# Kernel tuning notes

Measured on AMD Instinct MI355X. Metric: run time of the kernel, lower is better.

Reference implementation:

```python
import jax, jax.numpy as jnp
import numpy as np

D_MODEL = 512
D_ALPHA = 100
D_PH = 80
SCALE = 1.0 / np.sqrt(D_MODEL)


def gru_cell(x, h, Wih, Whh, bih, bhh):
    # PyTorch GRU gate order: r, z, n
    gi = x @ Wih.T + bih
    gh = h @ Whh.T + bhh
    ir, iz, inn = jnp.split(gi, 3, axis=-1)
    hr, hz, hn = jnp.split(gh, 3, axis=-1)
    r = jax.nn.sigmoid(ir + hr)
    z = jax.nn.sigmoid(iz + hz)
    n = jnp.tanh(inn + r * hn)
    return (1.0 - z) * n + z * h


def attend(q, k, v):
    # q: [B,D], k/v: [B,L,D]
    scores = jnp.einsum('bd,bld->bl', q, k) * SCALE
    a = jax.nn.softmax(scores, axis=-1)  # [B,L]
    o = jnp.einsum('bl,bld->bd', a, v)
    return a, o


def setup_inputs() -> dict:
    key = jax.random.key(0)
    ks = jax.random.split(key, 25)
    D = D_MODEL

    def u(k, shape, fan):
        return jax.random.uniform(k, shape, jnp.float32, -1.0, 1.0) / np.sqrt(fan)

    inp = {
        'text': jax.random.randint(ks[0], (256, 128), 0, D_ALPHA),
        'tgt': jax.random.randint(ks[1], (256, 64), 0, D_PH),
        'E_alpha': jax.random.normal(ks[2], (D_ALPHA, D), jnp.float32),
        'enc_Wih_f': u(ks[3], (3 * D, D), D),
        'enc_Whh_f': u(ks[4], (3 * D, D), D),
        'enc_bih_f': u(ks[5], (3 * D,), D),
        'enc_bhh_f': u(ks[6], (3 * D,), D),
        'enc_Wih_b': u(ks[7], (3 * D, D), D),
        'enc_Whh_b': u(ks[8], (3 * D, D), D),
        'enc_bih_b': u(ks[9], (3 * D,), D),
        'enc_bhh_b': u(ks[10], (3 * D,), D),
        'hpost_W': u(ks[11], (D, 2 * D), 2 * D),
        'hpost_b': u(ks[12], (D,), 2 * D),
        'wk_W': u(ks[13], (D, 2 * D), 2 * D),
        'wk_b': u(ks[14], (D,), 2 * D),
        'wv_W': u(ks[15], (D, 2 * D), 2 * D),
        'wv_b': u(ks[16], (D,), 2 * D),
        'E_ph': jax.random.normal(ks[17], (D_PH, D), jnp.float32),
        'dec_Wih': u(ks[18], (3 * D, 2 * D), 2 * D),
        'dec_Whh': u(ks[19], (3 * D, D), D),
        'dec_bih': u(ks[20], (3 * D,), D),
        'dec_bhh': u(ks[21], (3 * D,), D),
        'post_W': u(ks[22], (D_PH, D), D),
        'post_b': u(ks[23], (D_PH,), D),
    }
    return inp


def reference(text, tgt, E_alpha, enc_Wih_f, enc_Whh_f, enc_bih_f, enc_bhh_f,
              enc_Wih_b, enc_Whh_b, enc_bih_b, enc_bhh_b, hpost_W, hpost_b,
              wk_W, wk_b, wv_W, wv_b, E_ph, dec_Wih, dec_Whh, dec_bih,
              dec_bhh, post_W, post_b):
    B, LT = text.shape
    LP = tgt.shape[1]

    # ---- Encoder: bidirectional single-layer GRU (eval: dropout = identity)
    emb = E_alpha[text]                     # [B,LT,D]
    xs = jnp.swapaxes(emb, 0, 1)            # [LT,B,D]
    h0 = jnp.zeros((B, D_MODEL), emb.dtype)

    def mk_step(Wih, Whh, bih, bhh):
        def step(h, x):
            h2 = gru_cell(x, h, Wih, Whh, bih, bhh)
            return h2, h2
        return step

    hF, ysF = jax.lax.scan(mk_step(enc_Wih_f, enc_Whh_f, enc_bih_f, enc_bhh_f), h0, xs)
    hB, ysB = jax.lax.scan(mk_step(enc_Wih_b, enc_Whh_b, enc_bih_b, enc_bhh_b), h0, xs[::-1])
    ysB = ysB[::-1]
    enc_o = jnp.swapaxes(jnp.concatenate([ysF, ysB], axis=-1), 0, 1)  # [B,LT,2D]
    h = jnp.tanh(jnp.concatenate([hF, hB], axis=-1) @ hpost_W.T + hpost_b)  # [B,D]

    k = enc_o @ wk_W.T + wk_b               # [B,LT,D]
    v = enc_o @ wv_W.T + wv_b               # [B,LT,D]

    # ---- initial attention from encoder hidden; eval-mode first token is argmax
    # over tgt[:,0] reshaped to [B,1,1], i.e. always index 0.
    a_sl0, a_o0 = attend(h, k, v)
    dec_i0 = jnp.zeros((B,), jnp.int32)

    def dstep(carry, _):
        hh, a_o, a_sl, dec_i = carry
        e = E_ph[dec_i]                                  # [B,D]
        x = gru_cell(jnp.concatenate([e, a_o], axis=-1), hh,
                     dec_Wih, dec_Whh, dec_bih, dec_bhh)  # [B,D]
        o = x @ post_W.T + post_b                         # [B,D_PH]
        n_sl, n_o = attend(x, k, v)
        nxt = jnp.argmax(o, axis=-1).astype(jnp.int32)
        return (x, n_o, n_sl, nxt), (a_sl, o)

    _, (attn_t, res_t) = jax.lax.scan(dstep, (h, a_o0, a_sl0, dec_i0), None, length=LP)
    attn = jnp.swapaxes(attn_t, 0, 1)        # [B,LP,LT]
    res = jnp.swapaxes(res_t, 0, 1)          # [B,LP,D_PH]
    return attn, res
```

## Files before the change

### kernel.cpp

```cpp
#include <hip/hip_runtime.h>
#include <math.h>

#define B   256
#define LT  128
#define LP  64
#define DM  512
#define D3  1536
#define DPH 80
#define SCALE_F 0.044194173824159216f

__device__ __forceinline__ float dot4(float4 a, float4 b) {
    return a.x*b.x + a.y*b.y + a.z*b.z + a.w*b.w;
}
__device__ __forceinline__ float sigmoidf_(float x) {
    return 1.0f / (1.0f + expf(-x));
}

__global__ __launch_bounds__(256) void precompG_kernel(
    const float* __restrict__ Emb, const float* __restrict__ W,
    const float* __restrict__ bias, float* __restrict__ G,
    int wstride, int woff)
{
    const int n  = blockIdx.x * 256 + threadIdx.x;
    const int r0 = blockIdx.y * 4;
    __shared__ float es[4][DM];
    for (int i = threadIdx.x; i < 4 * DM; i += 256)
        es[i >> 9][i & 511] = Emb[(r0 + (i >> 9)) * DM + (i & 511)];
    __syncthreads();
    float acc[4] = {0.f, 0.f, 0.f, 0.f};
    const float* wr = &W[(size_t)n * wstride + woff];
    for (int j = 0; j < DM; j += 4) {
        float4 w4 = *(const float4*)&wr[j];
        #pragma unroll
        for (int rr = 0; rr < 4; ++rr) {
            float4 e4 = *(const float4*)&es[rr][j];
            acc[rr] += dot4(e4, w4);
        }
    }
    float bv = bias[n];
    #pragma unroll
    for (int rr = 0; rr < 4; ++rr)
        G[(r0 + rr) * D3 + n] = acc[rr] + bv;
}

__global__ __launch_bounds__(256) void enc_step_kernel(
    const float* __restrict__ Gf, const float* __restrict__ Gb,
    const float* __restrict__ Whh_f, const float* __restrict__ Whh_b,
    const float* __restrict__ bhh_f, const float* __restrict__ bhh_b,
    const int* __restrict__ text,
    const float* __restrict__ hF_in, float* __restrict__ hF_out,
    const float* __restrict__ hB_in, float* __restrict__ hB_out,
    float* __restrict__ E,
    int s)
{
    const int dir = blockIdx.z;
    const int t   = (dir == 0) ? s : (LT - 1 - s);
    const int yoff = (dir == 0) ? 0 : DM;
    const float* G   = (dir == 0) ? Gf    : Gb;
    const float* Whh = (dir == 0) ? Whh_f : Whh_b;
    const float* bhh = (dir == 0) ? bhh_f : bhh_b;
    const float* hin = (dir == 0) ? hF_in : hB_in;
    float* hout      = (dir == 0) ? hF_out : hB_out;

    __shared__ float As[2][16][36];
    __shared__ float Bs[2][96][36];

    const int tid = threadIdx.x;
    const int jj  = tid & 15;
    const int bb  = tid >> 4;
    const int jtile = blockIdx.x * 32;
    const int btile = blockIdx.y * 16;

    float acc[2][3];
    #pragma unroll
    for (int js = 0; js < 2; ++js)
        #pragma unroll
        for (int g = 0; g < 3; ++g) acc[js][g] = 0.f;

    const int lrow = tid >> 3;
    const int lcol = (tid & 7) * 4;

    int wrow[3];
    #pragma unroll
    for (int rr = 0; rr < 3; ++rr) {
        int brow = lrow + rr * 32;
        wrow[rr] = (brow >> 5) * DM + jtile + (brow & 31);
    }

    float4 rA = make_float4(0.f,0.f,0.f,0.f);
    if (tid < 128)
        rA = *(const float4*)&hin[(btile + lrow) * DM + lcol];
    float4 rB0 = *(const float4*)&Whh[(size_t)wrow[0] * DM + lcol];
    float4 rB1 = *(const float4*)&Whh[(size_t)wrow[1] * DM + lcol];
    float4 rB2 = *(const float4*)&Whh[(size_t)wrow[2] * DM + lcol];

    int buf = 0;
    for (int k = 0; k < 16; ++k) {
        if (tid < 128)
            *(float4*)&As[buf][lrow][lcol] = rA;
        *(float4*)&Bs[buf][lrow][lcol]      = rB0;
        *(float4*)&Bs[buf][lrow + 32][lcol] = rB1;
        *(float4*)&Bs[buf][lrow + 64][lcol] = rB2;
        __syncthreads();
        if (k < 15) {
            const int k0 = (k + 1) * 32;
            if (tid < 128)
                rA = *(const float4*)&hin[(btile + lrow) * DM + k0 + lcol];
            rB0 = *(const float4*)&Whh[(size_t)wrow[0] * DM + k0 + lcol];
            rB1 = *(const float4*)&Whh[(size_t)wrow[1] * DM + k0 + lcol];
            rB2 = *(const float4*)&Whh[(size_t)wrow[2] * DM + k0 + lcol];
        }
        #pragma unroll
        for (int c4 = 0; c4 < 8; ++c4) {
            float4 av = *(float4*)&As[buf][bb][c4 * 4];
            float4 bv[2][3];
            #pragma unroll
            for (int js = 0; js < 2; ++js)
                #pragma unroll
                for (int g = 0; g < 3; ++g)
                    bv[js][g] = *(float4*)&Bs[buf][g * 32 + jj + 16 * js][c4 * 4];
            #pragma unroll
            for (int js = 0; js < 2; ++js)
                #pragma unroll
                for (int g = 0; g < 3; ++g)
                    acc[js][g] += dot4(av, bv[js][g]);
        }
        buf ^= 1;
    }

    const int b = btile + bb;
    const int c = text[b * LT + t];
    #pragma unroll
    for (int js = 0; js < 2; ++js) {
        const int j = jtile + jj + 16 * js;
        float hr = acc[js][0] + bhh[j];
        float hz = acc[js][1] + bhh[DM + j];
        float hn = acc[js][2] + bhh[2 * DM + j];
        float r = sigmoidf_(G[c * D3 + j] + hr);
        float z = sigmoidf_(G[c * D3 + DM + j] + hz);
        float n = tanhf(G[c * D3 + 2 * DM + j] + r * hn);
        float hp = hin[b * DM + j];
        float hv = (1.f - z) * n + z * hp;
        hout[b * DM + j] = hv;
        E[(size_t)(b * LT + t) * 1024 + yoff + j] = hv;
    }
}

__global__ __launch_bounds__(256) void kv_chunk_kernel(
    const float* __restrict__ E,
    const float* __restrict__ wk, const float* __restrict__ wv,
    const float* __restrict__ kb, const float* __restrict__ vb,
    float* __restrict__ T, int r0)
{
    __shared__ float As[64][36];
    __shared__ float Bk[64][36];
    __shared__ float Bv[64][36];
    const int tid = threadIdx.x;
    const int nn = tid & 15, bb = tid >> 4;
    const int ntile = blockIdx.x * 64;
    const int mtile = blockIdx.y * 64;

    float ak[4][4], av_[4][4];
    #pragma unroll
    for (int m = 0; m < 4; ++m)
        #pragma unroll
        for (int i = 0; i < 4; ++i) { ak[m][i] = 0.f; av_[m][i] = 0.f; }

    const int lrow = tid >> 3;
    const int lcol = (tid & 7) * 4;

    for (int k0 = 0; k0 < 1024; k0 += 32) {
        __syncthreads();
        *(float4*)&As[lrow][lcol] =
            *(const float4*)&E[(size_t)(r0 + mtile + lrow) * 1024 + k0 + lcol];
        *(float4*)&As[lrow + 32][lcol] =
            *(const float4*)&E[(size_t)(r0 + mtile + lrow + 32) * 1024 + k0 + lcol];
        *(float4*)&Bk[lrow][lcol] =
            *(const float4*)&wk[(ntile + lrow) * 1024 + k0 + lcol];
        *(float4*)&Bk[lrow + 32][lcol] =
            *(const float4*)&wk[(ntile + lrow + 32) * 1024 + k0 + lcol];
        *(float4*)&Bv[lrow][lcol] =
            *(const float4*)&wv[(ntile + lrow) * 1024 + k0 + lcol];
        *(float4*)&Bv[lrow + 32][lcol] =
            *(const float4*)&wv[(ntile + lrow + 32) * 1024 + k0 + lcol];
        __syncthreads();
        #pragma unroll
        for (int c4 = 0; c4 < 8; ++c4) {
            float4 a4[4], k4[4], v4[4];
            #pragma unroll
            for (int m = 0; m < 4; ++m) a4[m] = *(float4*)&As[bb + 16 * m][c4 * 4];
            #pragma unroll
            for (int i = 0; i < 4; ++i) {
                k4[i] = *(float4*)&Bk[nn + 16 * i][c4 * 4];
                v4[i] = *(float4*)&Bv[nn + 16 * i][c4 * 4];
            }
            #pragma unroll
            for (int m = 0; m < 4; ++m)
                #pragma unroll
                for (int i = 0; i < 4; ++i) {
                    ak[m][i]  += dot4(a4[m], k4[i]);
                    av_[m][i] += dot4(a4[m], v4[i]);
                }
        }
    }
    #pragma unroll
    for (int m = 0; m < 4; ++m) {
        const int lm = mtile + bb + 16 * m;
        #pragma unroll
        for (int i = 0; i < 4; ++i) {
            const int gn = ntile + nn + 16 * i;
            T[(size_t)lm * 1024 + gn]       = ak[m][i]  + kb[gn];
            T[(size_t)lm * 1024 + DM + gn]  = av_[m][i] + vb[gn];
        }
    }
}

__global__ __launch_bounds__(256) void copy4_kernel(
    float4* __restrict__ dst, const float4* __restrict__ src, int n4)
{
    int i = blockIdx.x * 256 + threadIdx.x;
    const int stride = gridDim.x * 256;
    for (; i < n4; i += stride) dst[i] = src[i];
}

__global__ __launch_bounds__(256) void hpost_kernel(
    const float* __restrict__ hF, const float* __restrict__ hB,
    const float* __restrict__ W, const float* __restrict__ bias,
    float* __restrict__ out)
{
    const int b = blockIdx.x;
    __shared__ float as_[1024];
    for (int i = threadIdx.x; i < DM; i += 256) {
        as_[i]      = hF[b * DM + i];
        as_[DM + i] = hB[b * DM + i];
    }
    __syncthreads();
    for (int n = threadIdx.x; n < DM; n += 256) {
        const float* wr = &W[n * 1024];
        float acc = 0.f;
        for (int j = 0; j < 1024; j += 4)
            acc += dot4(*(const float4*)&as_[j], *(const float4*)&wr[j]);
        out[b * DM + n] = tanhf(acc + bias[n]);
    }
}

__global__ __launch_bounds__(256) void dec_step_kernel(
    const float* __restrict__ Gd,
    const float* __restrict__ dec_Wih, const float* __restrict__ dec_Whh,
    const float* __restrict__ bhh,
    const int* __restrict__ dec_i,
    const float* __restrict__ a_o,
    const float* __restrict__ h_in, float* __restrict__ h_out)
{
    __shared__ float As[2][8][36];
    __shared__ float Bs[2][96][36];
    const int tid = threadIdx.x;
    const int jj = tid & 15;
    const int js = (tid >> 4) & 1;
    const int bb = tid >> 5;
    const int jtile = blockIdx.x * 32;
    const int btile = blockIdx.y * 8;

    float acc[4];
    #pragma unroll
    for (int g = 0; g < 4; ++g) acc[g] = 0.f;

    const int lrow = tid >> 3;
    const int lcol = (tid & 7) * 4;

    int wrow[3];
    #pragma unroll
    for (int rr = 0; rr < 3; ++rr) {
        int brow = lrow + rr * 32;
        wrow[rr] = (brow >> 5) * DM + jtile + (brow & 31);
    }

    float4 rA = make_float4(0.f,0.f,0.f,0.f), rB0, rB1, rB2;
    if (tid < 64)
        rA = *(const float4*)&a_o[(btile + lrow) * DM + lcol];
    rB0 = *(const float4*)&dec_Wih[(size_t)wrow[0] * 1024 + DM + lcol];
    rB1 = *(const float4*)&dec_Wih[(size_t)wrow[1] * 1024 + DM + lcol];
    rB2 = *(const float4*)&dec_Wih[(size_t)wrow[2] * 1024 + DM + lcol];

    int buf = 0;
    for (int kk = 0; kk < 32; ++kk) {
        const int phase = kk >> 4;
        if (tid < 64)
            *(float4*)&As[buf][lrow][lcol] = rA;
        *(float4*)&Bs[buf][lrow][lcol]      = rB0;
        *(float4*)&Bs[buf][lrow + 32][lcol] = rB1;
        *(float4*)&Bs[buf][lrow + 64][lcol] = rB2;
        __syncthreads();
        if (kk < 31) {
            const int nk = kk + 1;
            const int np = nk >> 4;
            const int k0 = (nk & 15) * 32;
            if (tid < 64) {
                const float* Aptr = (np == 0) ? a_o : h_in;
                rA = *(const float4*)&Aptr[(btile + lrow) * DM + k0 + lcol];
            }
            if (np == 0) {
                rB0 = *(const float4*)&dec_Wih[(size_t)wrow[0] * 1024 + DM + k0 + lcol];
                rB1 = *(const float4*)&dec_Wih[(size_t)wrow[1] * 1024 + DM + k0 + lcol];
                rB2 = *(const float4*)&dec_Wih[(size_t)wrow[2] * 1024 + DM + k0 + lcol];
            } else {
                rB0 = *(const float4*)&dec_Whh[(size_t)wrow[0] * DM + k0 + lcol];
                rB1 = *(const float4*)&dec_Whh[(size_t)wrow[1] * DM + k0 + lcol];
                rB2 = *(const float4*)&dec_Whh[(size_t)wrow[2] * DM + k0 + lcol];
            }
        }
        #pragma unroll
        for (int c4 = 0; c4 < 8; ++c4) {
            float4 av = *(float4*)&As[buf][bb][c4 * 4];
            float4 bv[3];
            #pragma unroll
            for (int g = 0; g < 3; ++g)
                bv[g] = *(float4*)&Bs[buf][g * 32 + jj + 16 * js][c4 * 4];
            acc[0]         += dot4(av, bv[0]);
            acc[1]         += dot4(av, bv[1]);
            acc[2 + phase] += dot4(av, bv[2]);
        }
        buf ^= 1;
    }

    const int b = btile + bb;
    const int c = dec_i[b];
    const int j = jtile + jj + 16 * js;
    float r = sigmoidf_(Gd[c * D3 + j] + bhh[j] + acc[0]);
    float z = sigmoidf_(Gd[c * D3 + DM + j] + bhh[DM + j] + acc[1]);
    float n = tanhf(Gd[c * D3 + 2 * DM + j] + acc[2]
                    + r * (acc[3] + bhh[2 * DM + j]));
    float hp = h_in[b * DM + j];
    h_out[b * DM + j] = (1.f - z) * n + z * hp;
}

__global__ __launch_bounds__(256) void dec_attend_post_kernel(
    const float* __restrict__ q,
    const float* __restrict__ EKV,
    const float* __restrict__ post_W, const float* __restrict__ post_b,
    float* __restrict__ attn, float* __restrict__ res,
    float* __restrict__ a_o, int* __restrict__ dec_i,
    int s, int attn_row, int do_post, int do_attn)
{
    const int b = blockIdx.x;
    const int tid = threadIdx.x;
    __shared__ float qs[DM];
    __shared__ float part[256];
    __shared__ float sarr[LT];
    __shared__ float red[2];
    __shared__ float4 pvp[2][128];

    if (tid < 128)
        *(float4*)&qs[tid * 4] = *(const float4*)&q[b * DM + tid * 4];
    __syncthreads();

    if (do_post) {
        if (tid < DPH) {
            const float* wr = &post_W[tid * DM];
            float acc = 0.f;
            for (int d = 0; d < DM; d += 4)
                acc += dot4(*(const float4*)&qs[d], *(const float4*)&wr[d]);
            float lv = acc + post_b[tid];
            res[(b * LP + s) * DPH + tid] = lv;
            part[tid] = lv;
        }
        __syncthreads();
        if (tid == 0) {
            float best = part[0]; int bi = 0;
            for (int p = 1; p < DPH; ++p) {
                float vv = part[p];
                if (vv > best) { best = vv; bi = p; }
            }
            dec_i[b] = bi;
        }
        __syncthreads();
    }

    if (do_attn) {
        {
            const int r = tid & 127, half = tid >> 7;
            const float* kr = &EKV[(size_t)(b * LT + r) * 1024 + half * 256];
            const float* qh = &qs[half * 256];
            float p = 0.f;
            #pragma unroll
            for (int d = 0; d < 256; d += 4)
                p += dot4(*(const float4*)&qh[d], *(const float4*)&kr[d]);
            part[tid] = p;
        }
        __syncthreads();
        if (tid < LT) sarr[tid] = (part[tid] + part[tid + 128]) * SCALE_F;
        __syncthreads();
        if (tid < 64) {
            float m = fmaxf(sarr[tid], sarr[tid + 64]);
            #pragma unroll
            for (int off = 32; off > 0; off >>= 1)
                m = fmaxf(m, __shfl_xor(m, off));
            if (tid == 0) red[0] = m;
        }
        __syncthreads();
        const float smax = red[0];
        if (tid < LT) sarr[tid] = expf(sarr[tid] - smax);
        __syncthreads();
        if (tid < 64) {
            float ssum = sarr[tid] + sarr[tid + 64];
            #pragma unroll
            for (int off = 32; off > 0; off >>= 1)
                ssum += __shfl_xor(ssum, off);
            if (tid == 0) red[1] = ssum;
        }
        __syncthreads();
        const float inv = 1.0f / red[1];
        if (tid < LT) {
            float a = sarr[tid] * inv;
            sarr[tid] = a;
            attn[(size_t)(b * LP + attn_row) * LT + tid] = a;
        }
        __syncthreads();
        {
            const int d4 = tid & 127, half = tid >> 7;
            const float* vb0 = &EKV[(size_t)b * LT * 1024 + DM];
            float4 acc = make_float4(0.f, 0.f, 0.f, 0.f);
            const int l0 = half * 64;
            #pragma unroll 8
            for (int l = l0; l < l0 + 64; ++l) {
                float a = sarr[l];
                float4 v4 = *(const float4*)&vb0[(size_t)l * 1024 + d4 * 4];
                acc.x += a * v4.x; acc.y += a * v4.y;
                acc.z += a * v4.z; acc.w += a * v4.w;
            }
            pvp[half][d4] = acc;
        }
        __syncthreads();
        if (tid < 128) {
            float4 p0 = pvp[0][tid], p1 = pvp[1][tid];
            float4 o = make_float4(p0.x + p1.x, p0.y + p1.y,
                                   p0.z + p1.z, p0.w + p1.w);
            *(float4*)&a_o[b * DM + tid * 4] = o;
        }
    }
}

extern "C" void kernel_launch(void* const* d_in, const int* in_sizes, int n_in,
                              void* d_out, int out_size, void* d_ws, size_t ws_size,
                              hipStream_t stream)
{
    const int*   text    = (const int*)d_in[0];
    const float* E_alpha = (const float*)d_in[2];
    const float* Wih_f   = (const float*)d_in[3];
    const float* Whh_f   = (const float*)d_in[4];
    const float* bih_f   = (const float*)d_in[5];
    const float* bhh_f   = (const float*)d_in[6];
    const float* Wih_b   = (const float*)d_in[7];
    const float* Whh_b   = (const float*)d_in[8];
    const float* bih_b   = (const float*)d_in[9];
    const float* bhh_b   = (const float*)d_in[10];
    const float* hpost_W = (const float*)d_in[11];
    const float* hpost_b = (const float*)d_in[12];
    const float* wk_W    = (const float*)d_in[13];
    const float* wk_b    = (const float*)d_in[14];
    const float* wv_W    = (const float*)d_in[15];
    const float* wv_b    = (const float*)d_in[16];
    const float* E_ph    = (const float*)d_in[17];
    const float* dec_Wih = (const float*)d_in[18];
    const float* dec_Whh = (const float*)d_in[19];
    const float* dec_bih = (const float*)d_in[20];
    const float* dec_bhh = (const float*)d_in[21];
    const float* post_W  = (const float*)d_in[22];
    const float* post_b  = (const float*)d_in[23];

    float* ws = (float*)d_ws;
    float* Gf  = ws;
    float* Gb  = Gf  + 153600;
    float* Gd  = Gb  + 153600;
    float* hF0 = Gd  + 122880;
    float* hF1 = hF0 + 131072;
    float* hB0 = hF1 + 131072;
    float* hB1 = hB0 + 131072;
    float* hd0 = hB1 + 131072;
    float* hd1 = hd0 + 131072;
    float* a_o = hd1 + 131072;
    int*   dec_i = (int*)(a_o + 131072);
    float* E   = a_o + 131072 + 512;
    float* T   = E + 33554432;

    hipMemsetAsync(hF0, 0, 131072 * sizeof(float), stream);
    hipMemsetAsync(hB0, 0, 131072 * sizeof(float), stream);
    hipMemsetAsync(dec_i, 0, B * sizeof(int), stream);

    precompG_kernel<<<dim3(6, 25), 256, 0, stream>>>(E_alpha, Wih_f, bih_f, Gf, DM, 0);
    precompG_kernel<<<dim3(6, 25), 256, 0, stream>>>(E_alpha, Wih_b, bih_b, Gb, DM, 0);
    precompG_kernel<<<dim3(6, 20), 256, 0, stream>>>(E_ph, dec_Wih, dec_bih, Gd, 1024, 0);

    for (int s = 0; s < LT; ++s) {
        const float* fin = (s & 1) ? hF1 : hF0;
        float*       fou = (s & 1) ? hF0 : hF1;
        const float* bin = (s & 1) ? hB1 : hB0;
        float*       bou = (s & 1) ? hB0 : hB1;
        enc_step_kernel<<<dim3(16, 16, 2), 256, 0, stream>>>(
            Gf, Gb, Whh_f, Whh_b, bhh_f, bhh_b, text,
            fin, fou, bin, bou, E, s);
    }

    for (int c = 0; c < 2; ++c) {
        const int r0 = c * 16384;
        kv_chunk_kernel<<<dim3(8, 256), 256, 0, stream>>>(
            E, wk_W, wv_W, wk_b, wv_b, T, r0);
        copy4_kernel<<<dim3(4096), 256, 0, stream>>>(
            (float4*)(E + (size_t)r0 * 1024), (const float4*)T,
            16384 * 1024 / 4);
    }

    hpost_kernel<<<dim3(B), 256, 0, stream>>>(hF0, hB0, hpost_W, hpost_b, hd0);

    float* attn = (float*)d_out;
    float* res  = attn + (size_t)B * LP * LT;

    dec_attend_post_kernel<<<dim3(B), 256, 0, stream>>>(
        hd0, E, post_W, post_b, attn, res, a_o, dec_i,
        0, 0, 0, 1);

    for (int s = 0; s < LP; ++s) {
        const float* hin = (s & 1) ? hd1 : hd0;
        float*       hou = (s & 1) ? hd0 : hd1;
        dec_step_kernel<<<dim3(16, 32), 256, 0, stream>>>(
            Gd, dec_Wih, dec_Whh, dec_bhh, dec_i, a_o, hin, hou);
        dec_attend_post_kernel<<<dim3(B), 256, 0, stream>>>(
            hou, E, post_W, post_b, attn, res, a_o, dec_i,
            s, s + 1, 1, (s < LP - 1) ? 1 : 0);
    }
}
```

Measured before the change: 10.54 ms.

## Replace per-step encoder/decoder launches with persistent kernels using grid barriers

```diff
diff --git a/kernel.cpp b/kernel.cpp
--- a/kernel.cpp
+++ b/kernel.cpp
@@ -14,6 +14,19 @@
 }
 __device__ __forceinline__ float sigmoidf_(float x) {
     return 1.0f / (1.0f + expf(-x));
+}
+
+__device__ __forceinline__ void grid_barrier(int* bar, int nblk) {
+    __syncthreads();
+    if (threadIdx.x == 0) {
+        int ticket = __hip_atomic_fetch_add(bar, 1, __ATOMIC_ACQ_REL,
+                                            __HIP_MEMORY_SCOPE_AGENT);
+        int target = (ticket / nblk + 1) * nblk;
+        while (__hip_atomic_load(bar, __ATOMIC_ACQUIRE,
+                                 __HIP_MEMORY_SCOPE_AGENT) < target)
+            __builtin_amdgcn_s_sleep(8);
+    }
+    __syncthreads();
 }
 
 __global__ __launch_bounds__(256) void precompG_kernel(
@@ -43,106 +56,124 @@
         G[(r0 + rr) * D3 + n] = acc[rr] + bv;
 }
 
-__global__ __launch_bounds__(256) void enc_step_kernel(
+__global__ __launch_bounds__(256, 1) void enc_persist_kernel(
     const float* __restrict__ Gf, const float* __restrict__ Gb,
     const float* __restrict__ Whh_f, const float* __restrict__ Whh_b,
     const float* __restrict__ bhh_f, const float* __restrict__ bhh_b,
     const int* __restrict__ text,
-    const float* __restrict__ hF_in, float* __restrict__ hF_out,
-    const float* __restrict__ hB_in, float* __restrict__ hB_out,
+    float* __restrict__ hF0, float* __restrict__ hF1,
+    float* __restrict__ hB0, float* __restrict__ hB1,
     float* __restrict__ E,
-    int s)
-{
-    const int dir = blockIdx.z;
-    const int t   = (dir == 0) ? s : (LT - 1 - s);
-    const int yoff = (dir == 0) ? 0 : DM;
-    const float* G   = (dir == 0) ? Gf    : Gb;
-    const float* Whh = (dir == 0) ? Whh_f : Whh_b;
-    const float* bhh = (dir == 0) ? bhh_f : bhh_b;
-    const float* hin = (dir == 0) ? hF_in : hB_in;
-    float* hout      = (dir == 0) ? hF_out : hB_out;
-
-    __shared__ float As[2][16][36];
-    __shared__ float Bs[2][96][36];
-
-    const int tid = threadIdx.x;
-    const int jj  = tid & 15;
-    const int bb  = tid >> 4;
-    const int jtile = blockIdx.x * 32;
-    const int btile = blockIdx.y * 16;
-
-    float acc[2][3];
-    #pragma unroll
-    for (int js = 0; js < 2; ++js)
-        #pragma unroll
-        for (int g = 0; g < 3; ++g) acc[js][g] = 0.f;
-
-    const int lrow = tid >> 3;
-    const int lcol = (tid & 7) * 4;
-
-    int wrow[3];
-    #pragma unroll
-    for (int rr = 0; rr < 3; ++rr) {
-        int brow = lrow + rr * 32;
-        wrow[rr] = (brow >> 5) * DM + jtile + (brow & 31);
-    }
-
-    float4 rA = make_float4(0.f,0.f,0.f,0.f);
-    if (tid < 128)
-        rA = *(const float4*)&hin[(btile + lrow) * DM + lcol];
-    float4 rB0 = *(const float4*)&Whh[(size_t)wrow[0] * DM + lcol];
-    float4 rB1 = *(const float4*)&Whh[(size_t)wrow[1] * DM + lcol];
-    float4 rB2 = *(const float4*)&Whh[(size_t)wrow[2] * DM + lcol];
-
-    int buf = 0;
-    for (int k = 0; k < 16; ++k) {
-        if (tid < 128)
-            *(float4*)&As[buf][lrow][lcol] = rA;
-        *(float4*)&Bs[buf][lrow][lcol]      = rB0;
-        *(float4*)&Bs[buf][lrow + 32][lcol] = rB1;
-        *(float4*)&Bs[buf][lrow + 64][lcol] = rB2;
-        __syncthreads();
-        if (k < 15) {
-            const int k0 = (k + 1) * 32;
-            if (tid < 128)
-                rA = *(const float4*)&hin[(btile + lrow) * DM + k0 + lcol];
-            rB0 = *(const float4*)&Whh[(size_t)wrow[0] * DM + k0 + lcol];
-            rB1 = *(const float4*)&Whh[(size_t)wrow[1] * DM + k0 + lcol];
-            rB2 = *(const float4*)&Whh[(size_t)wrow[2] * DM + k0 + lcol];
-        }
-        #pragma unroll
-        for (int c4 = 0; c4 < 8; ++c4) {
-            float4 av = *(float4*)&As[buf][bb][c4 * 4];
-            float4 bv[2][3];
-            #pragma unroll
-            for (int js = 0; js < 2; ++js)
+    const float* __restrict__ hpost_W, const float* __restrict__ hpost_b,
+    float* __restrict__ hd0, int* __restrict__ bar)
+{
+    __shared__ float Wl[48][516];
+    __shared__ float As[2][64][36];
+    __shared__ float xs[1024];
+    __shared__ float bl[48];
+
+    const int tid  = threadIdx.x;
+    const int blk  = blockIdx.x;
+    const int dir  = blk & 1;
+    const int jblk = (blk >> 1) & 31;
+    const int bblk = blk >> 6;
+    const int jtile = jblk * 16;
+    const int btile = bblk * 64;
+
+    const float* G   = dir ? Gb : Gf;
+    const float* Whh = dir ? Whh_b : Whh_f;
+    const float* bhh = dir ? bhh_b : bhh_f;
+    float* h0 = dir ? hB0 : hF0;
+    float* h1 = dir ? hB1 : hF1;
+    const int yoff = dir ? DM : 0;
+
+    for (int i = tid; i < 48 * 128; i += 256) {
+        const int r = i >> 7, c = (i & 127) << 2;
+        const int g = r >> 4, j = jtile + (r & 15);
+        *(float4*)&Wl[r][c] =
+            *(const float4*)&Whh[(size_t)(g * DM + j) * DM + c];
+    }
+    if (tid < 48) bl[tid] = bhh[(tid >> 4) * DM + jtile + (tid & 15)];
+    __syncthreads();
+
+    const int jj   = tid & 15;
+    const int rg   = tid >> 4;
+    const int lrow = tid >> 2;
+    const int lcol = (tid & 3) * 8;
+
+    for (int s = 0; s < LT; ++s) {
+        const int t = dir ? (LT - 1 - s) : s;
+        const float* hin = (s & 1) ? h1 : h0;
+        float* hout      = (s & 1) ? h0 : h1;
+
+        float acc[4][3];
+        #pragma unroll
+        for (int m = 0; m < 4; ++m) {
+            acc[m][0] = 0.f; acc[m][1] = 0.f; acc[m][2] = 0.f;
+        }
+
+        float4 rA0 = *(const float4*)&hin[(btile + lrow) * DM + lcol];
+        float4 rA1 = *(const float4*)&hin[(btile + lrow) * DM + lcol + 4];
+        int buf = 0;
+        for (int kc = 0; kc < 16; ++kc) {
+            *(float4*)&As[buf][lrow][lcol]     = rA0;
+            *(float4*)&As[buf][lrow][lcol + 4] = rA1;
+            __syncthreads();
+            if (kc < 15) {
+                const int k0 = (kc + 1) * 32;
+                rA0 = *(const float4*)&hin[(btile + lrow) * DM + k0 + lcol];
+                rA1 = *(const float4*)&hin[(btile + lrow) * DM + k0 + lcol + 4];
+            }
+            const int kb = kc * 32;
+            #pragma unroll
+            for (int c4 = 0; c4 < 8; ++c4) {
+                float4 bv0 = *(float4*)&Wl[jj][kb + c4 * 4];
+                float4 bv1 = *(float4*)&Wl[16 + jj][kb + c4 * 4];
+                float4 bv2 = *(float4*)&Wl[32 + jj][kb + c4 * 4];
                 #pragma unroll
-                for (int g = 0; g < 3; ++g)
-                    bv[js][g] = *(float4*)&Bs[buf][g * 32 + jj + 16 * js][c4 * 4];
-            #pragma unroll
-            for (int js = 0; js < 2; ++js)
-                #pragma unroll
-                for (int g = 0; g < 3; ++g)
-                    acc[js][g] += dot4(av, bv[js][g]);
-        }
-        buf ^= 1;
-    }
-
-    const int b = btile + bb;
-    const int c = text[b * LT + t];
-    #pragma unroll
-    for (int js = 0; js < 2; ++js) {
-        const int j = jtile + jj + 16 * js;
-        float hr = acc[js][0] + bhh[j];
-        float hz = acc[js][1] + bhh[DM + j];
-        float hn = acc[js][2] + bhh[2 * DM + j];
-        float r = sigmoidf_(G[c * D3 + j] + hr);
-        float z = sigmoidf_(G[c * D3 + DM + j] + hz);
-        float n = tanhf(G[c * D3 + 2 * DM + j] + r * hn);
-        float hp = hin[b * DM + j];
-        float hv = (1.f - z) * n + z * hp;
-        hout[b * DM + j] = hv;
-        E[(size_t)(b * LT + t) * 1024 + yoff + j] = hv;
+                for (int m = 0; m < 4; ++m) {
+                    float4 av = *(float4*)&As[buf][rg * 4 + m][c4 * 4];
+                    acc[m][0] += dot4(av, bv0);
+                    acc[m][1] += dot4(av, bv1);
+                    acc[m][2] += dot4(av, bv2);
+                }
+            }
+            buf ^= 1;
+        }
+
+        const int j = jtile + jj;
+        #pragma unroll
+        for (int m = 0; m < 4; ++m) {
+            const int b = btile + rg * 4 + m;
+            const int c = text[b * LT + t];
+            float hr = acc[m][0] + bl[jj];
+            float hz = acc[m][1] + bl[16 + jj];
+            float hn = acc[m][2] + bl[32 + jj];
+            float r = sigmoidf_(G[c * D3 + j] + hr);
+            float z = sigmoidf_(G[c * D3 + DM + j] + hz);
+            float n = tanhf(G[c * D3 + 2 * DM + j] + r * hn);
+            float hp = hin[b * DM + j];
+            float hv = (1.f - z) * n + z * hp;
+            hout[b * DM + j] = hv;
+            E[(size_t)(b * LT + t) * 1024 + yoff + j] = hv;
+        }
+        grid_barrier(bar, 256);
+    }
+
+    {
+        const int b = blk;
+        for (int i = tid; i < DM; i += 256) {
+            xs[i]      = hF0[b * DM + i];
+            xs[DM + i] = hB0[b * DM + i];
+        }
+        __syncthreads();
+        for (int n = tid; n < DM; n += 256) {
+            const float* wr = &hpost_W[n * 1024];
+            float acc = 0.f;
+            for (int jx = 0; jx < 1024; jx += 4)
+                acc += dot4(*(const float4*)&xs[jx], *(const float4*)&wr[jx]);
+            hd0[b * DM + n] = tanhf(acc + hpost_b[n]);
+        }
     }
 }
 
@@ -223,133 +254,14 @@
     for (; i < n4; i += stride) dst[i] = src[i];
 }
 
-__global__ __launch_bounds__(256) void hpost_kernel(
-    const float* __restrict__ hF, const float* __restrict__ hB,
-    const float* __restrict__ W, const float* __restrict__ bias,
-    float* __restrict__ out)
-{
-    const int b = blockIdx.x;
-    __shared__ float as_[1024];
-    for (int i = threadIdx.x; i < DM; i += 256) {
-        as_[i]      = hF[b * DM + i];
-        as_[DM + i] = hB[b * DM + i];
-    }
-    __syncthreads();
-    for (int n = threadIdx.x; n < DM; n += 256) {
-        const float* wr = &W[n * 1024];
-        float acc = 0.f;
-        for (int j = 0; j < 1024; j += 4)
-            acc += dot4(*(const float4*)&as_[j], *(const float4*)&wr[j]);
-        out[b * DM + n] = tanhf(acc + bias[n]);
-    }
-}
-
-__global__ __launch_bounds__(256) void dec_step_kernel(
-    const float* __restrict__ Gd,
-    const float* __restrict__ dec_Wih, const float* __restrict__ dec_Whh,
-    const float* __restrict__ bhh,
-    const int* __restrict__ dec_i,
-    const float* __restrict__ a_o,
-    const float* __restrict__ h_in, float* __restrict__ h_out)
-{
-    __shared__ float As[2][8][36];
-    __shared__ float Bs[2][96][36];
-    const int tid = threadIdx.x;
-    const int jj = tid & 15;
-    const int js = (tid >> 4) & 1;
-    const int bb = tid >> 5;
-    const int jtile = blockIdx.x * 32;
-    const int btile = blockIdx.y * 8;
-
-    float acc[4];
-    #pragma unroll
-    for (int g = 0; g < 4; ++g) acc[g] = 0.f;
-
-    const int lrow = tid >> 3;
-    const int lcol = (tid & 7) * 4;
-
-    int wrow[3];
-    #pragma unroll
-    for (int rr = 0; rr < 3; ++rr) {
-        int brow = lrow + rr * 32;
-        wrow[rr] = (brow >> 5) * DM + jtile + (brow & 31);
-    }
-
-    float4 rA = make_float4(0.f,0.f,0.f,0.f), rB0, rB1, rB2;
-    if (tid < 64)
-        rA = *(const float4*)&a_o[(btile + lrow) * DM + lcol];
-    rB0 = *(const float4*)&dec_Wih[(size_t)wrow[0] * 1024 + DM + lcol];
-    rB1 = *(const float4*)&dec_Wih[(size_t)wrow[1] * 1024 + DM + lcol];
-    rB2 = *(const float4*)&dec_Wih[(size_t)wrow[2] * 1024 + DM + lcol];
-
-    int buf = 0;
-    for (int kk = 0; kk < 32; ++kk) {
-        const int phase = kk >> 4;
-        if (tid < 64)
-            *(float4*)&As[buf][lrow][lcol] = rA;
-        *(float4*)&Bs[buf][lrow][lcol]      = rB0;
-        *(float4*)&Bs[buf][lrow + 32][lcol] = rB1;
-        *(float4*)&Bs[buf][lrow + 64][lcol] = rB2;
-        __syncthreads();
-        if (kk < 31) {
-            const int nk = kk + 1;
-            const int np = nk >> 4;
-            const int k0 = (nk & 15) * 32;
-            if (tid < 64) {
-                const float* Aptr = (np == 0) ? a_o : h_in;
-                rA = *(const float4*)&Aptr[(btile + lrow) * DM + k0 + lcol];
-            }
-            if (np == 0) {
-                rB0 = *(const float4*)&dec_Wih[(size_t)wrow[0] * 1024 + DM + k0 + lcol];
-                rB1 = *(const float4*)&dec_Wih[(size_t)wrow[1] * 1024 + DM + k0 + lcol];
-                rB2 = *(const float4*)&dec_Wih[(size_t)wrow[2] * 1024 + DM + k0 + lcol];
-            } else {
-                rB0 = *(const float4*)&dec_Whh[(size_t)wrow[0] * DM + k0 + lcol];
-                rB1 = *(const float4*)&dec_Whh[(size_t)wrow[1] * DM + k0 + lcol];
-                rB2 = *(const float4*)&dec_Whh[(size_t)wrow[2] * DM + k0 + lcol];
-            }
-        }
-        #pragma unroll
-        for (int c4 = 0; c4 < 8; ++c4) {
-            float4 av = *(float4*)&As[buf][bb][c4 * 4];
-            float4 bv[3];
-            #pragma unroll
-            for (int g = 0; g < 3; ++g)
-                bv[g] = *(float4*)&Bs[buf][g * 32 + jj + 16 * js][c4 * 4];
-            acc[0]         += dot4(av, bv[0]);
-            acc[1]         += dot4(av, bv[1]);
-            acc[2 + phase] += dot4(av, bv[2]);
-        }
-        buf ^= 1;
-    }
-
-    const int b = btile + bb;
-    const int c = dec_i[b];
-    const int j = jtile + jj + 16 * js;
-    float r = sigmoidf_(Gd[c * D3 + j] + bhh[j] + acc[0]);
-    float z = sigmoidf_(Gd[c * D3 + DM + j] + bhh[DM + j] + acc[1]);
-    float n = tanhf(Gd[c * D3 + 2 * DM + j] + acc[2]
-                    + r * (acc[3] + bhh[2 * DM + j]));
-    float hp = h_in[b * DM + j];
-    h_out[b * DM + j] = (1.f - z) * n + z * hp;
-}
-
-__global__ __launch_bounds__(256) void dec_attend_post_kernel(
-    const float* __restrict__ q,
-    const float* __restrict__ EKV,
+__device__ __forceinline__ void attend_body(
+    int b, int tid, const float* __restrict__ q, const float* __restrict__ EKV,
     const float* __restrict__ post_W, const float* __restrict__ post_b,
     float* __restrict__ attn, float* __restrict__ res,
     float* __restrict__ a_o, int* __restrict__ dec_i,
-    int s, int attn_row, int do_post, int do_attn)
-{
-    const int b = blockIdx.x;
-    const int tid = threadIdx.x;
-    __shared__ float qs[DM];
-    __shared__ float part[256];
-    __shared__ float sarr[LT];
-    __shared__ float red[2];
-    __shared__ float4 pvp[2][128];
-
+    int s, int attn_row, int do_post, int do_attn,
+    float* qs, float* part, float* sarr, float* red, float4 (*pvp)[128])
+{
     if (tid < 128)
         *(float4*)&qs[tid * 4] = *(const float4*)&q[b * DM + tid * 4];
     __syncthreads();
@@ -361,7 +273,7 @@
             for (int d = 0; d < DM; d += 4)
                 acc += dot4(*(const float4*)&qs[d], *(const float4*)&wr[d]);
             float lv = acc + post_b[tid];
-            res[(b * LP + s) * DPH + tid] = lv;
+            res[(size_t)(b * LP + s) * DPH + tid] = lv;
             part[tid] = lv;
         }
         __syncthreads();
@@ -437,6 +349,121 @@
                                    p0.z + p1.z, p0.w + p1.w);
             *(float4*)&a_o[b * DM + tid * 4] = o;
         }
+    }
+}
+
+__global__ __launch_bounds__(256, 1) void dec_persist_kernel(
+    const float* __restrict__ Gd,
+    const float* __restrict__ dec_Wih, const float* __restrict__ dec_Whh,
+    const float* __restrict__ dec_bhh,
+    const float* __restrict__ EKV,
+    const float* __restrict__ post_W, const float* __restrict__ post_b,
+    float* __restrict__ attn, float* __restrict__ res,
+    float* __restrict__ a_o, int* __restrict__ dec_i,
+    float* __restrict__ hd0, float* __restrict__ hd1,
+    int* __restrict__ bar)
+{
+    __shared__ float Wi[24][516];
+    __shared__ float Wh[24][516];
+    __shared__ float As[2][64][36];
+    __shared__ float bl[24];
+    __shared__ float qs[DM];
+    __shared__ float part[256];
+    __shared__ float sarr[LT];
+    __shared__ float red[2];
+    __shared__ float4 pvp[2][128];
+
+    const int tid  = threadIdx.x;
+    const int blk  = blockIdx.x;
+    const int jblk = blk & 63;
+    const int bblk = blk >> 6;
+    const int jtile = jblk * 8;
+    const int btile = bblk * 64;
+
+    for (int i = tid; i < 24 * 128; i += 256) {
+        const int r = i >> 7, c = (i & 127) << 2;
+        const int g = r >> 3, j = jtile + (r & 7);
+        *(float4*)&Wi[r][c] =
+            *(const float4*)&dec_Wih[(size_t)(g * DM + j) * 1024 + DM + c];
+        *(float4*)&Wh[r][c] =
+            *(const float4*)&dec_Whh[(size_t)(g * DM + j) * DM + c];
+    }
+    if (tid < 24) bl[tid] = dec_bhh[(tid >> 3) * DM + jtile + (tid & 7)];
+    __syncthreads();
+
+    attend_body(blk, tid, hd0, EKV, post_W, post_b, attn, res, a_o, dec_i,
+                0, 0, 0, 1, qs, part, sarr, red, pvp);
+    grid_barrier(bar, 256);
+
+    const int jj   = tid & 7;
+    const int rg   = tid >> 3;
+    const int lrow = tid >> 2;
+    const int lcol = (tid & 3) * 8;
+
+    for (int s = 0; s < LP; ++s) {
+        const float* hin = (s & 1) ? hd1 : hd0;
+        float* hout      = (s & 1) ? hd0 : hd1;
+
+        float acc[2][4];
+        #pragma unroll
+        for (int m = 0; m < 2; ++m)
+            #pragma unroll
+            for (int g = 0; g < 4; ++g) acc[m][g] = 0.f;
+
+        #pragma unroll
+        for (int ph = 0; ph < 2; ++ph) {
+            const float* Aptr = (ph == 0) ? a_o : hin;
+            const float (*W)[516] = (ph == 0) ? Wi : Wh;
+
+            float4 rA0 = *(const float4*)&Aptr[(btile + lrow) * DM + lcol];
+            float4 rA1 = *(const float4*)&Aptr[(btile + lrow) * DM + lcol + 4];
+            int buf = 0;
+            for (int kc = 0; kc < 16; ++kc) {
+                *(float4*)&As[buf][lrow][lcol]     = rA0;
+                *(float4*)&As[buf][lrow][lcol + 4] = rA1;
+                __syncthreads();
+                if (kc < 15) {
+                    const int k0 = (kc + 1) * 32;
+                    rA0 = *(const float4*)&Aptr[(btile + lrow) * DM + k0 + lcol];
+                    rA1 = *(const float4*)&Aptr[(btile + lrow) * DM + k0 + lcol + 4];
+                }
+                const int kb = kc * 32;
+                #pragma unroll
+                for (int c4 = 0; c4 < 8; ++c4) {
+                    float4 bv0 = *(float4*)&W[jj][kb + c4 * 4];
+                    float4 bv1 = *(float4*)&W[8 + jj][kb + c4 * 4];
+                    float4 bv2 = *(float4*)&W[16 + jj][kb + c4 * 4];
+                    #pragma unroll
+                    for (int m = 0; m < 2; ++m) {
+                        float4 av = *(float4*)&As[buf][rg * 2 + m][c4 * 4];
+                        acc[m][0]      += dot4(av, bv0);
+                        acc[m][1]      += dot4(av, bv1);
+                        acc[m][2 + ph] += dot4(av, bv2);
+                    }
+                }
+                buf ^= 1;
+            }
+            __syncthreads();
+        }
+
+        const int j = jtile + jj;
+        #pragma unroll
+        for (int m = 0; m < 2; ++m) {
+            const int b = btile + rg * 2 + m;
+            const int c = dec_i[b];
+            float r = sigmoidf_(Gd[c * D3 + j] + bl[jj] + acc[m][0]);
+            float z = sigmoidf_(Gd[c * D3 + DM + j] + bl[8 + jj] + acc[m][1]);
+            float n = tanhf(Gd[c * D3 + 2 * DM + j] + acc[m][2]
+                            + r * (acc[m][3] + bl[16 + jj]));
+            float hp = hin[b * DM + j];
+            hout[b * DM + j] = (1.f - z) * n + z * hp;
+        }
+        grid_barrier(bar, 256);
+
+        attend_body(blk, tid, hout, EKV, post_W, post_b, attn, res, a_o, dec_i,
+                    s, s + 1, 1, (s < LP - 1) ? 1 : 0,
+                    qs, part, sarr, red, pvp);
+        grid_barrier(bar, 256);
     }
 }
 
@@ -480,26 +507,21 @@
     float* hd1 = hd0 + 131072;
     float* a_o = hd1 + 131072;
     int*   dec_i = (int*)(a_o + 131072);
+    int*   bar   = dec_i + 256;
     float* E   = a_o + 131072 + 512;
     float* T   = E + 33554432;
 
     hipMemsetAsync(hF0, 0, 131072 * sizeof(float), stream);
     hipMemsetAsync(hB0, 0, 131072 * sizeof(float), stream);
-    hipMemsetAsync(dec_i, 0, B * sizeof(int), stream);
+    hipMemsetAsync(dec_i, 0, 258 * sizeof(int), stream);
 
     precompG_kernel<<<dim3(6, 25), 256, 0, stream>>>(E_alpha, Wih_f, bih_f, Gf, DM, 0);
     precompG_kernel<<<dim3(6, 25), 256, 0, stream>>>(E_alpha, Wih_b, bih_b, Gb, DM, 0);
     precompG_kernel<<<dim3(6, 20), 256, 0, stream>>>(E_ph, dec_Wih, dec_bih, Gd, 1024, 0);
 
-    for (int s = 0; s < LT; ++s) {
-        const float* fin = (s & 1) ? hF1 : hF0;
-        float*       fou = (s & 1) ? hF0 : hF1;
-        const float* bin = (s & 1) ? hB1 : hB0;
-        float*       bou = (s & 1) ? hB0 : hB1;
-        enc_step_kernel<<<dim3(16, 16, 2), 256, 0, stream>>>(
-            Gf, Gb, Whh_f, Whh_b, bhh_f, bhh_b, text,
-            fin, fou, bin, bou, E, s);
-    }
+    enc_persist_kernel<<<dim3(256), 256, 0, stream>>>(
+        Gf, Gb, Whh_f, Whh_b, bhh_f, bhh_b, text,
+        hF0, hF1, hB0, hB1, E, hpost_W, hpost_b, hd0, bar);
 
     for (int c = 0; c < 2; ++c) {
         const int r0 = c * 16384;
@@ -510,22 +532,10 @@
             16384 * 1024 / 4);
     }
 
-    hpost_kernel<<<dim3(B), 256, 0, stream>>>(hF0, hB0, hpost_W, hpost_b, hd0);
-
     float* attn = (float*)d_out;
     float* res  = attn + (size_t)B * LP * LT;
 
-    dec_attend_post_kernel<<<dim3(B), 256, 0, stream>>>(
-        hd0, E, post_W, post_b, attn, res, a_o, dec_i,
-        0, 0, 0, 1);
-
-    for (int s = 0; s < LP; ++s) {
-        const float* hin = (s & 1) ? hd1 : hd0;
-        float*       hou = (s & 1) ? hd0 : hd1;
-        dec_step_kernel<<<dim3(16, 32), 256, 0, stream>>>(
-            Gd, dec_Wih, dec_Whh, dec_bhh, dec_i, a_o, hin, hou);
-        dec_attend_post_kernel<<<dim3(B), 256, 0, stream>>>(
-            hou, E, post_W, post_b, attn, res, a_o, dec_i,
-            s, s + 1, 1, (s < LP - 1) ? 1 : 0);
-    }
-}
+    dec_persist_kernel<<<dim3(256), 256, 0, stream>>>(
+        Gd, dec_Wih, dec_Whh, dec_bhh, E, post_W, post_b,
+        attn, res, a_o, dec_i, hd0, hd1, bar + 1);
+}
```

Measured after the change: 16.04 ms. 52.2% more time.
